# Kernel tuning notes

Measured on AMD Instinct MI355X. Metric: run time of the kernel, lower is better.

## Reference

```python
import jax, jax.numpy as jnp
import numpy as np

# dims
B, S, D, H, NB = 2, 2048, 1024, 16, 32
DH = D // H          # 64 per-head dim
MLP = 4096
CLUSTER_SCORE = 0.1
LN_EPS = 1e-6


def _layernorm(x, g, b):
    mu = jnp.mean(x, axis=-1, keepdims=True)
    var = jnp.mean(jnp.square(x - mu), axis=-1, keepdims=True)
    return (x - mu) * jax.lax.rsqrt(var + LN_EPS) * g + b


def setup_inputs() -> dict:
    key = jax.random.key(0)
    ks = jax.random.split(key, 10)
    std = 0.02  # xl_init-style normal init scale
    return {
        "inputs": jax.random.normal(ks[0], (B, S, D), jnp.float32),
        "ln1_g": jnp.ones((D,), jnp.float32),
        "ln1_b": jnp.zeros((D,), jnp.float32),
        "Wq": jax.random.normal(ks[1], (D, H, DH), jnp.float32) * std,
        "Wk": jax.random.normal(ks[2], (D, H, DH), jnp.float32) * std,
        "Wv": jax.random.normal(ks[3], (D, H, DH), jnp.float32) * std,
        "Whq": jax.random.normal(ks[4], (H, DH, NB), jnp.float32) * std,
        "Whk": jax.random.normal(ks[5], (H, DH, NB), jnp.float32) * std,
        "Wo": jax.random.normal(ks[6], (H, DH, D), jnp.float32) * std,
        "ln2_g": jnp.ones((D,), jnp.float32),
        "ln2_b": jnp.zeros((D,), jnp.float32),
        "W1": jax.random.normal(ks[7], (D, MLP), jnp.float32) * std,
        "b1": jnp.zeros((MLP,), jnp.float32),
        "W2": jax.random.normal(ks[8], (MLP, D), jnp.float32) * std,
        "b2": jnp.zeros((D,), jnp.float32),
    }


def _lha_attention(x, Wq, Wk, Wv, Whq, Whk, Wo):
    # q,k,v: [B,S,H,DH]
    q = jnp.einsum("bsd,dhf->bshf", x, Wq)
    k = jnp.einsum("bsd,dhf->bshf", x, Wk)
    v = jnp.einsum("bsd,dhf->bshf", x, Wv)
    # learned-hash bucket assignment probabilities (lha_score_func='linear')
    qb = jax.nn.softmax(jnp.einsum("bshf,hfn->bshn", q, Whq), axis=-1)  # [B,S,H,NB]
    kb = jax.nn.softmax(jnp.einsum("bshf,hfn->bshn", k, Whk), axis=-1)
    # content scores + cluster (same-bucket) affinity term
    logits = jnp.einsum("bqhf,bkhf->bhqk", q, k) / jnp.sqrt(jnp.float32(DH))
    aff = jnp.einsum("bqhn,bkhn->bhqk", qb, kb)  # [B,H,S,S]
    logits = logits + CLUSTER_SCORE * aff
    attn = jax.nn.softmax(logits, axis=-1)
    out = jnp.einsum("bhqk,bkhf->bqhf", attn, v)
    out = jnp.einsum("bqhf,hfd->bqd", out, Wo)
    # auxiliary bucket load-balancing loss
    mq = jnp.mean(qb, axis=(0, 1))  # [H,NB]
    mk = jnp.mean(kb, axis=(0, 1))
    extra_loss = 0.5 * NB * (jnp.mean(jnp.sum(mq * mq, -1)) + jnp.mean(jnp.sum(mk * mk, -1)))
    return out, extra_loss


def reference(inputs, ln1_g, ln1_b, Wq, Wk, Wv, Whq, Whk, Wo,
              ln2_g, ln2_b, W1, b1, W2, b2):
    x = _layernorm(inputs, ln1_g, ln1_b)                      # pre-LN
    attn_out, extra_loss = _lha_attention(x, Wq, Wk, Wv, Whq, Whk, Wo)
    x = attn_out + inputs                                      # residual
    y = _layernorm(x, ln2_g, ln2_b)                            # pre-LN for MLP
    y = jax.nn.relu(jnp.einsum("bsd,dm->bsm", y, W1) + b1)
    y = jnp.einsum("bsm,md->bsd", y, W2) + b2
    return (x + y, extra_loss)
```

## Files before the change

kernel.cpp:

```cpp
#include <hip/hip_runtime.h>

typedef unsigned short u16;
typedef unsigned int u32;
typedef float f32x4 __attribute__((ext_vector_type(4)));
typedef short bf16x8 __attribute__((ext_vector_type(8)));

#define D_B 2
#define D_S 2048
#define D_D 1024
#define D_H 16
#define D_NB 32
#define D_DH 64
#define D_MLP 4096

__device__ __forceinline__ float bflo(u32 p) { union { u32 i; float f; } c; c.i = p << 16; return c.f; }
__device__ __forceinline__ float bfhi(u32 p) { union { u32 i; float f; } c; c.i = p & 0xffff0000u; return c.f; }
__device__ __forceinline__ u16 f2bf(float f) {
  union { float f; u32 i; } c; c.f = f;
  u32 x = c.i;
  u32 r = (x + 0x7fffu + ((x >> 16) & 1u)) >> 16;
  return (u16)r;
}
__device__ __forceinline__ u32 pack2(float lo, float hi) {
  return (u32)f2bf(lo) | ((u32)f2bf(hi) << 16);
}
__device__ __forceinline__ void unpack8(uint4 u, float* f) {
  f[0]=bflo(u.x); f[1]=bfhi(u.x); f[2]=bflo(u.y); f[3]=bfhi(u.y);
  f[4]=bflo(u.z); f[5]=bfhi(u.z); f[6]=bflo(u.w); f[7]=bfhi(u.w);
}
__device__ __forceinline__ bf16x8 scale_frag(uint4 u, float s) {
  float f[8]; unpack8(u, f);
  uint4 r;
  r.x = pack2(f[0]*s, f[1]*s); r.y = pack2(f[2]*s, f[3]*s);
  r.z = pack2(f[4]*s, f[5]*s); r.w = pack2(f[6]*s, f[7]*s);
  union { uint4 u; bf16x8 v; } c; c.u = r; return c.v;
}
__device__ __forceinline__ bf16x8 as_frag(uint4 u) {
  union { uint4 u; bf16x8 v; } c; c.u = u; return c.v;
}
__device__ __forceinline__ void gl_lds16(const u16* g, u16* l) {
  __builtin_amdgcn_global_load_lds((const __attribute__((address_space(1))) void*)g,
                                   (__attribute__((address_space(3))) void*)l, 16, 0, 0);
}

__device__ __forceinline__ void tr64(const float* __restrict__ W, u16* __restrict__ WT,
                                     int K, int N, int k0, int n0, int t) {
  __shared__ float tile[64][65];
  int tx = t & 15, ty = t >> 4;
  #pragma unroll
  for (int i = 0; i < 4; i++) {
    float4 v = *reinterpret_cast<const float4*>(W + (size_t)(k0 + ty * 4 + i) * N + n0 + tx * 4);
    tile[ty * 4 + i][tx * 4 + 0] = v.x;
    tile[ty * 4 + i][tx * 4 + 1] = v.y;
    tile[ty * 4 + i][tx * 4 + 2] = v.z;
    tile[ty * 4 + i][tx * 4 + 3] = v.w;
  }
  __syncthreads();
  #pragma unroll
  for (int i = 0; i < 4; i++) {
    int n = ty * 4 + i;
    uint2 o;
    o.x = pack2(tile[tx*4+0][n], tile[tx*4+1][n]);
    o.y = pack2(tile[tx*4+2][n], tile[tx*4+3][n]);
    *reinterpret_cast<uint2*>(WT + (size_t)(n0 + n) * K + k0 + tx * 4) = o;
  }
}

__global__ __launch_bounds__(256) void prep1_kernel(const float* __restrict__ Wq,
                                                    const float* __restrict__ Wk,
                                                    const float* __restrict__ Wv,
                                                    const float* __restrict__ Wo,
                                                    u16* __restrict__ wqkvT,
                                                    u16* __restrict__ woT,
                                                    float* __restrict__ mqmk) {
  int bid = blockIdx.x, t = threadIdx.x;
  if (bid >= 1024) {
    reinterpret_cast<float4*>(mqmk)[t] = make_float4(0.f, 0.f, 0.f, 0.f);
    return;
  }
  const float* W; u16* WT;
  int sub = bid & 255;
  int k0 = (sub >> 4) * 64, n0 = (sub & 15) * 64;
  if (bid < 256)      { W = Wq; WT = wqkvT; }
  else if (bid < 512) { W = Wk; WT = wqkvT + 1024 * 1024; }
  else if (bid < 768) { W = Wv; WT = wqkvT + 2048 * 1024; }
  else                { W = Wo; WT = woT; }
  tr64(W, WT, 1024, 1024, k0, n0, t);
}

__global__ __launch_bounds__(256) void prep2_kernel(const float* __restrict__ W1,
                                                    const float* __restrict__ W2,
                                                    u16* __restrict__ w1T,
                                                    u16* __restrict__ w2T) {
  int bid = blockIdx.x, t = threadIdx.x;
  if (bid < 1024) {
    int n0 = (bid & 63) * 64, k0 = (bid >> 6) * 64;
    tr64(W1, w1T, 1024, 4096, k0, n0, t);
  } else {
    int i = bid - 1024;
    int n0 = (i & 15) * 64, k0 = (i >> 4) * 64;
    tr64(W2, w2T, 4096, 1024, k0, n0, t);
  }
}

__global__ __launch_bounds__(256) void ln_kernel(const float* __restrict__ x,
                                                 const float* __restrict__ g,
                                                 const float* __restrict__ bta,
                                                 u16* __restrict__ out) {
  int row = blockIdx.x, t = threadIdx.x;
  float4 v = reinterpret_cast<const float4*>(x + (size_t)row * D_D)[t];
  float s = v.x + v.y + v.z + v.w;
  float q = v.x*v.x + v.y*v.y + v.z*v.z + v.w*v.w;
  #pragma unroll
  for (int o = 32; o; o >>= 1) { s += __shfl_down(s, o); q += __shfl_down(q, o); }
  __shared__ float rs[4], rq[4];
  if ((t & 63) == 0) { rs[t >> 6] = s; rq[t >> 6] = q; }
  __syncthreads();
  s = rs[0] + rs[1] + rs[2] + rs[3];
  q = rq[0] + rq[1] + rq[2] + rq[3];
  float mu   = s * (1.0f / 1024.0f);
  float var  = fmaxf(q * (1.0f / 1024.0f) - mu * mu, 0.0f);
  float rstd = rsqrtf(var + 1e-6f);
  float4 gg = reinterpret_cast<const float4*>(g)[t];
  float4 bb = reinterpret_cast<const float4*>(bta)[t];
  float o0 = (v.x - mu) * rstd * gg.x + bb.x;
  float o1 = (v.y - mu) * rstd * gg.y + bb.y;
  float o2 = (v.z - mu) * rstd * gg.z + bb.z;
  float o3 = (v.w - mu) * rstd * gg.w + bb.w;
  uint2 w; w.x = pack2(o0, o1); w.y = pack2(o2, o3);
  reinterpret_cast<uint2*>(out + (size_t)row * D_D)[t] = w;
}

__global__ __launch_bounds__(256, 2) void gemm_bt(const u16* __restrict__ A,
                                                  const u16* __restrict__ Bt,
                                                  u16* __restrict__ Cq,
                                                  u16* __restrict__ Ck,
                                                  u16* __restrict__ Cv,
                                                  int M, int N, int K, int ldb) {
  __shared__ u16 As[128 * 32];
  __shared__ u16 Bs[128 * 32];
  const int t = threadIdx.x, w = t >> 6, lane = t & 63;
  const int quad = lane >> 4, l16 = lane & 15;
  const int m0 = blockIdx.y * 128, n0 = blockIdx.x * 128;
  const int wm = (w >> 1) * 64, wn = (w & 1) * 64;

  f32x4 acc[4][4];
  #pragma unroll
  for (int i = 0; i < 4; i++)
    #pragma unroll
    for (int n = 0; n < 4; n++) acc[i][n] = (f32x4){0.f, 0.f, 0.f, 0.f};

  const int srow = lane >> 2, scol = (lane & 3) * 8;
  const u16* ag0 = A  + (size_t)(m0 + w * 32 + srow) * K + scol;
  const u16* ag1 = ag0 + (size_t)16 * K;
  const u16* bg0 = Bt + (size_t)(n0 + w * 32 + srow) * ldb + scol;
  const u16* bg1 = bg0 + (size_t)16 * ldb;
  u16* al0 = As + w * 1024;
  u16* bl0 = Bs + w * 1024;

  for (int k0 = 0; k0 < K; k0 += 32) {
    gl_lds16(ag0 + k0, al0);
    gl_lds16(ag1 + k0, al0 + 512);
    gl_lds16(bg0 + k0, bl0);
    gl_lds16(bg1 + k0, bl0 + 512);
    __syncthreads();
    bf16x8 af[4], bf[4];
    #pragma unroll
    for (int i = 0; i < 4; i++)
      af[i] = *reinterpret_cast<const bf16x8*>(As + (wm + i * 16 + l16) * 32 + quad * 8);
    #pragma unroll
    for (int n = 0; n < 4; n++)
      bf[n] = *reinterpret_cast<const bf16x8*>(Bs + (wn + n * 16 + l16) * 32 + quad * 8);
    #pragma unroll
    for (int i = 0; i < 4; i++)
      #pragma unroll
      for (int n = 0; n < 4; n++)
        acc[i][n] = __builtin_amdgcn_mfma_f32_16x16x32_bf16(af[i], bf[n], acc[i][n], 0, 0, 0);
    __syncthreads();
  }

  #pragma unroll
  for (int i = 0; i < 4; i++) {
    #pragma unroll
    for (int r = 0; r < 4; r++) {
      const int m = m0 + wm + i * 16 + quad * 4 + r;
      #pragma unroll
      for (int nt = 0; nt < 4; nt++) {
        const int n = n0 + wn + nt * 16 + l16;
        float v = acc[i][nt][r];
        const int sel = n >> 10, nn = n & 1023;
        const int h = nn >> 6, f = nn & 63;
        const int b = m >> 11, s = m & 2047;
        const size_t bh = (size_t)(b * D_H + h);
        if (sel == 0)      Cq[(bh * D_S + s) * 96 + f] = f2bf(v);
        else if (sel == 1) Ck[(bh * D_S + s) * 96 + f] = f2bf(v);
        else               Cv[(bh * 64 + f) * D_S + s] = f2bf(v);
      }
    }
  }
}

__global__ __launch_bounds__(256, 2) void gemm_bt64(const u16* __restrict__ A,
                                                    const u16* __restrict__ Bt,
                                                    const float* __restrict__ bias,
                                                    const float* __restrict__ resid,
                                                    void* __restrict__ C,
                                                    int M, int N, int K, int ldb,
                                                    int do_relu, int out_f32) {
  __shared__ u16 As[64 * 32];
  __shared__ u16 Bs[128 * 32];
  const int t = threadIdx.x, w = t >> 6, lane = t & 63;
  const int quad = lane >> 4, l16 = lane & 15;
  const int m0 = blockIdx.y * 64, n0 = blockIdx.x * 128;
  const int wm = (w >> 1) * 32, wn = (w & 1) * 64;

  f32x4 acc[2][4];
  #pragma unroll
  for (int i = 0; i < 2; i++)
    #pragma unroll
    for (int n = 0; n < 4; n++) acc[i][n] = (f32x4){0.f, 0.f, 0.f, 0.f};

  const int srow = lane >> 2, scol = (lane & 3) * 8;
  const u16* ag0 = A  + (size_t)(m0 + w * 16 + srow) * K + scol;
  const u16* bg0 = Bt + (size_t)(n0 + w * 32 + srow) * ldb + scol;
  const u16* bg1 = bg0 + (size_t)16 * ldb;
  u16* al0 = As + w * 512;
  u16* bl0 = Bs + w * 1024;

  for (int k0 = 0; k0 < K; k0 += 32) {
    gl_lds16(ag0 + k0, al0);
    gl_lds16(bg0 + k0, bl0);
    gl_lds16(bg1 + k0, bl0 + 512);
    __syncthreads();
    bf16x8 af[2], bf[4];
    #pragma unroll
    for (int i = 0; i < 2; i++)
      af[i] = *reinterpret_cast<const bf16x8*>(As + (wm + i * 16 + l16) * 32 + quad * 8);
    #pragma unroll
    for (int n = 0; n < 4; n++)
      bf[n] = *reinterpret_cast<const bf16x8*>(Bs + (wn + n * 16 + l16) * 32 + quad * 8);
    #pragma unroll
    for (int i = 0; i < 2; i++)
      #pragma unroll
      for (int n = 0; n < 4; n++)
        acc[i][n] = __builtin_amdgcn_mfma_f32_16x16x32_bf16(af[i], bf[n], acc[i][n], 0, 0, 0);
    __syncthreads();
  }

  #pragma unroll
  for (int i = 0; i < 2; i++) {
    #pragma unroll
    for (int r = 0; r < 4; r++) {
      const int m = m0 + wm + i * 16 + quad * 4 + r;
      #pragma unroll
      for (int nt = 0; nt < 4; nt++) {
        const int n = n0 + wn + nt * 16 + l16;
        float v = acc[i][nt][r];
        if (bias)    v += bias[n];
        if (do_relu) v  = fmaxf(v, 0.0f);
        if (resid)   v += resid[(size_t)m * N + n];
        if (out_f32) reinterpret_cast<float*>(C)[(size_t)m * N + n] = v;
        else         reinterpret_cast<u16*>(C)[(size_t)m * N + n]   = f2bf(v);
      }
    }
  }
}

__global__ __launch_bounds__(256) void bucket2_kernel(u16* __restrict__ qp,
                                                      const float* __restrict__ Whq,
                                                      float* __restrict__ mq,
                                                      u16* __restrict__ kp,
                                                      const float* __restrict__ Whk,
                                                      float* __restrict__ mk) {
  const int bx = blockIdx.x;
  const int side = bx >> 8;
  u16* P        = side ? kp  : qp;
  const float* Wh = side ? Whk : Whq;
  float* acc    = side ? mk  : mq;
  const float sscale = side ? 1.0f : 0.1f;
  const int id = bx & 255;
  const int bh = id >> 3, chunk = id & 7;
  const int h = bh & 15;
  const int t = threadIdx.x, w = t >> 6, lane = t & 63;
  const int rsub = lane >> 5;
  const int b = lane & 31;

  __shared__ float WhL[32 * 65];
  __shared__ float qs[4][2][64];
  __shared__ float accL[32];

  #pragma unroll
  for (int i = 0; i < 8; i++) {
    int idx = t * 8 + i;
    WhL[(idx & 31) * 65 + (idx >> 5)] = Wh[h * 2048 + idx];
  }
  if (t < 32) accL[t] = 0.f;
  __syncthreads();

  float whr[64];
  #pragma unroll
  for (int i = 0; i < 16; i++) {
    float4 v = *reinterpret_cast<const float4*>(&WhL[b * 65 + i * 4]);
    whr[i*4+0] = v.x; whr[i*4+1] = v.y; whr[i*4+2] = v.z; whr[i*4+3] = v.w;
  }

  float racc = 0.f;
  const int row0 = bh * 2048 + chunk * 256;
  for (int it = 0; it < 32; it++) {
    const int rr = row0 + it * 8 + w * 2 + rsub;
    u16* qrow = P + (size_t)rr * 96;
    u32 u = *reinterpret_cast<const u32*>(qrow + b * 2);
    *reinterpret_cast<float2*>(&qs[w][rsub][b * 2]) = make_float2(bflo(u), bfhi(u));
    float s0 = 0.f, s1 = 0.f, s2 = 0.f, s3 = 0.f;
    #pragma unroll
    for (int i = 0; i < 16; i++) {
      float4 qv = *reinterpret_cast<const float4*>(&qs[w][rsub][i * 4]);
      s0 = fmaf(qv.x, whr[i*4+0], s0);
      s1 = fmaf(qv.y, whr[i*4+1], s1);
      s2 = fmaf(qv.z, whr[i*4+2], s2);
      s3 = fmaf(qv.w, whr[i*4+3], s3);
    }
    float l = (s0 + s1) + (s2 + s3);
    float m = l;
    m = fmaxf(m, __shfl_xor(m, 1));  m = fmaxf(m, __shfl_xor(m, 2));
    m = fmaxf(m, __shfl_xor(m, 4));  m = fmaxf(m, __shfl_xor(m, 8));
    m = fmaxf(m, __shfl_xor(m, 16));
    float e = __expf(fminf(l - m, 0.0f));
    float ss = e;
    ss += __shfl_xor(ss, 1);  ss += __shfl_xor(ss, 2);
    ss += __shfl_xor(ss, 4);  ss += __shfl_xor(ss, 8);
    ss += __shfl_xor(ss, 16);
    float p = e / fmaxf(ss, 1e-20f);
    qrow[64 + b] = f2bf(p * sscale);
    racc += p;
  }
  atomicAdd(&accL[b], racc);
  __syncthreads();
  if (t < 32) atomicAdd(&acc[h * D_NB + t], accL[t]);
}

__global__ __launch_bounds__(128, 2) void attn_kernel(const u16* __restrict__ qp,
                                                      const u16* __restrict__ kp,
                                                      const u16* __restrict__ vt,
                                                      u16* __restrict__ out) {
  const int bh = blockIdx.y;
  const int s0 = blockIdx.x * 64;
  const int h = bh & 15, b = bh >> 4;
  const int t = threadIdx.x, w = t >> 6, lane = t & 63;
  const int quad = lane >> 4, l16 = lane & 15;

  __shared__ u16 Ks[64 * 104];
  __shared__ u16 Vs[64 * 72];
  __shared__ u16 Ps[2][32 * 72];

  bf16x8 Qf[2][3];
  #pragma unroll
  for (int m = 0; m < 2; m++) {
    const u16* qr = qp + ((size_t)bh * D_S + s0 + w * 32 + m * 16 + l16) * 96;
    #pragma unroll
    for (int kg = 0; kg < 3; kg++) {
      uint4 u = *reinterpret_cast<const uint4*>(qr + kg * 32 + quad * 8);
      Qf[m][kg] = (kg < 2) ? scale_frag(u, 0.125f) : as_frag(u);
    }
  }

  f32x4 Oa[2][4];
  float lp[2][4];
  #pragma unroll
  for (int m = 0; m < 2; m++)
    #pragma unroll
    for (int f = 0; f < 4; f++) Oa[m][f] = (f32x4){0.f,0.f,0.f,0.f};
  #pragma unroll
  for (int m = 0; m < 2; m++)
    #pragma unroll
    for (int r = 0; r < 4; r++) lp[m][r] = 0.f;

  const int srow = t >> 1, shalf = t & 1;
  const u16* kgp = kp + ((size_t)bh * D_S + srow) * 96 + shalf * 48;
  const u16* vgp = vt + ((size_t)bh * 64 + srow) * D_S + shalf * 32;
  u16* kds = Ks + srow * 104 + shalf * 48;
  u16* vds = Vs + srow * 72 + shalf * 32;

  for (int kt = 0; kt < 32; kt++) {
    __syncthreads();
    {
      const u16* kg_ = kgp + (size_t)kt * 64 * 96;
      #pragma unroll
      for (int j = 0; j < 6; j++)
        *reinterpret_cast<uint4*>(kds + j * 8) = *reinterpret_cast<const uint4*>(kg_ + j * 8);
      const u16* vg_ = vgp + kt * 64;
      #pragma unroll
      for (int j = 0; j < 4; j++)
        *reinterpret_cast<uint4*>(vds + j * 8) = *reinterpret_cast<const uint4*>(vg_ + j * 8);
    }
    __syncthreads();

    f32x4 S[2][4];
    #pragma unroll
    for (int m = 0; m < 2; m++)
      #pragma unroll
      for (int n = 0; n < 4; n++) S[m][n] = (f32x4){0.f,0.f,0.f,0.f};
    #pragma unroll
    for (int n = 0; n < 4; n++) {
      bf16x8 Bk[3];
      #pragma unroll
      for (int kg = 0; kg < 3; kg++)
        Bk[kg] = *reinterpret_cast<const bf16x8*>(Ks + (n * 16 + l16) * 104 + kg * 32 + quad * 8);
      #pragma unroll
      for (int m = 0; m < 2; m++)
        #pragma unroll
        for (int kg = 0; kg < 3; kg++)
          S[m][n] = __builtin_amdgcn_mfma_f32_16x16x32_bf16(Qf[m][kg], Bk[kg], S[m][n], 0, 0, 0);
    }

    #pragma unroll
    for (int m = 0; m < 2; m++) {
      u16* pw = Ps[w] + (m * 16 + quad * 4) * 72 + l16;
      #pragma unroll
      for (int r = 0; r < 4; r++) {
        float es = 0.f;
        #pragma unroll
        for (int n = 0; n < 4; n++) {
          float e = __expf(fminf(S[m][n][r], 30.0f));
          es += e;
          pw[r * 72 + n * 16] = f2bf(e);
        }
        lp[m][r] += es;
      }
    }
    asm volatile("s_waitcnt lgkmcnt(0)" ::: "memory");

    #pragma unroll
    for (int m = 0; m < 2; m++) {
      bf16x8 Pa[2];
      #pragma unroll
      for (int kg = 0; kg < 2; kg++)
        Pa[kg] = *reinterpret_cast<const bf16x8*>(Ps[w] + (m * 16 + l16) * 72 + kg * 32 + quad * 8);
      #pragma unroll
      for (int f = 0; f < 4; f++)
        #pragma unroll
        for (int kg = 0; kg < 2; kg++) {
          bf16x8 Bv = *reinterpret_cast<const bf16x8*>(Vs + (f * 16 + l16) * 72 + kg * 32 + quad * 8);
          Oa[m][f] = __builtin_amdgcn_mfma_f32_16x16x32_bf16(Pa[kg], Bv, Oa[m][f], 0, 0, 0);
        }
    }
  }

  #pragma unroll
  for (int m = 0; m < 2; m++)
    #pragma unroll
    for (int r = 0; r < 4; r++) {
      float v = lp[m][r];
      v += __shfl_xor(v, 1); v += __shfl_xor(v, 2);
      v += __shfl_xor(v, 4); v += __shfl_xor(v, 8);
      float inv = 1.0f / fmaxf(v, 1e-20f);
      int qrow = s0 + w * 32 + m * 16 + quad * 4 + r;
      #pragma unroll
      for (int f = 0; f < 4; f++)
        out[((size_t)(b * D_S + qrow) * D_H + h) * 64 + f * 16 + l16] = f2bf(Oa[m][f][r] * inv);
    }
}

__global__ __launch_bounds__(256) void loss_kernel(const float* __restrict__ mq,
                                                   const float* __restrict__ mk,
                                                   float* __restrict__ out) {
  int t = threadIdx.x;
  float s = 0.0f;
  for (int i = t; i < 512; i += 256) {
    float a = mq[i] * (1.0f / 4096.0f);
    float c = mk[i] * (1.0f / 4096.0f);
    s += a * a + c * c;
  }
  #pragma unroll
  for (int o = 32; o; o >>= 1) s += __shfl_xor(s, o);
  __shared__ float r[4];
  if ((t & 63) == 0) r[t >> 6] = s;
  __syncthreads();
  if (t == 0) out[0] = r[0] + r[1] + r[2] + r[3];
}

extern "C" void kernel_launch(void* const* d_in, const int* in_sizes, int n_in,
                              void* d_out, int out_size, void* d_ws, size_t ws_size,
                              hipStream_t stream) {
  const float* inp  = (const float*)d_in[0];
  const float* ln1g = (const float*)d_in[1];
  const float* ln1b = (const float*)d_in[2];
  const float* Wq   = (const float*)d_in[3];
  const float* Wk   = (const float*)d_in[4];
  const float* Wv   = (const float*)d_in[5];
  const float* Whq  = (const float*)d_in[6];
  const float* Whk  = (const float*)d_in[7];
  const float* Wo   = (const float*)d_in[8];
  const float* ln2g = (const float*)d_in[9];
  const float* ln2b = (const float*)d_in[10];
  const float* W1   = (const float*)d_in[11];
  const float* b1   = (const float*)d_in[12];
  const float* W2   = (const float*)d_in[13];
  const float* b2   = (const float*)d_in[14];
  float* out = (float*)d_out;

  char* w = (char*)d_ws;
  u16* wqkvT = (u16*)(w + 0);
  u16* woT   = (u16*)(w + 6291456);
  u16* qp    = (u16*)(w + 8388608);
  u16* kp    = (u16*)(w + 20971520);
  u16* xhat  = (u16*)(w + 33554432);
  u16* attnb = xhat;
  float* mq  = (float*)(w + 41943040);
  float* mk  = mq + 512;
  u16* yhat  = (u16*)(w + 0);
  u16* w1T   = (u16*)(w + 8388608);
  u16* w2T   = (u16*)(w + 16777216);
  u16* h1    = (u16*)(w + 25165824);
  u16* vt    = (u16*)d_out;

  prep1_kernel<<<dim3(1025), dim3(256), 0, stream>>>(Wq, Wk, Wv, Wo, wqkvT, woT, mq);
  ln_kernel<<<dim3(4096), dim3(256), 0, stream>>>(inp, ln1g, ln1b, xhat);
  gemm_bt<<<dim3(24, 32), dim3(256), 0, stream>>>(xhat, wqkvT, qp, kp, vt, 4096, 3072, 1024, 1024);
  bucket2_kernel<<<dim3(512), dim3(256), 0, stream>>>(qp, Whq, mq, kp, Whk, mk);
  attn_kernel<<<dim3(32, 32), dim3(128), 0, stream>>>(qp, kp, vt, attnb);
  prep2_kernel<<<dim3(2048), dim3(256), 0, stream>>>(W1, W2, w1T, w2T);
  gemm_bt64<<<dim3(8, 64), dim3(256), 0, stream>>>(attnb, woT, nullptr, inp,
                                                   out, 4096, 1024, 1024, 1024, 0, 1);
  ln_kernel<<<dim3(4096), dim3(256), 0, stream>>>(out, ln2g, ln2b, yhat);
  gemm_bt64<<<dim3(16, 64), dim3(256), 0, stream>>>(yhat, w1T, b1, nullptr,
                                                    h1, 4096, 2048, 1024, 1024, 1, 0);
  gemm_bt64<<<dim3(8, 64), dim3(256), 0, stream>>>(h1, w2T, b2, out,
                                                   out, 4096, 1024, 2048, 4096, 0, 1);
  gemm_bt64<<<dim3(16, 64), dim3(256), 0, stream>>>(yhat, w1T + (size_t)2048 * 1024, b1 + 2048, nullptr,
                                                    h1, 4096, 2048, 1024, 1024, 1, 0);
  gemm_bt64<<<dim3(8, 64), dim3(256), 0, stream>>>(h1, w2T + 2048, nullptr, out,
                                                   out, 4096, 1024, 2048, 4096, 0, 1);
  loss_kernel<<<dim3(1), dim3(256), 0, stream>>>(mq, mk, out + 4194304);
}
```

Baseline: 487.1 us.

## Split attention KV range across two warp pairs and merge partial outputs

The attention block grows from 128 to 256 threads. Two extra waves process the second half of the key/value sequence in parallel with the first, using double K/V shared buffers, and their partial accumulators and row sums are merged through shared memory at the end. The P staging buffer gets a padded, swizzled layout to reduce LDS bank conflicts, and the bf16 conversion for P uses a cheaper round-half-up instead of round-to-nearest-even. The aim is more waves in flight per block to hide latency, at the cost of more shared memory per block, a final reduction step, and slightly different rounding of P.

Result: no change. 484.8 us (-0.5%).

```diff
diff --git a/kernel.cpp b/kernel.cpp
--- a/kernel.cpp
+++ b/kernel.cpp
@@ -20,6 +20,10 @@
   u32 x = c.i;
   u32 r = (x + 0x7fffu + ((x >> 16) & 1u)) >> 16;
   return (u16)r;
+}
+__device__ __forceinline__ u16 f2bf_fast(float f) {
+  union { float f; u32 i; } c; c.f = f;
+  return (u16)((c.i + 0x8000u) >> 16);
 }
 __device__ __forceinline__ u32 pack2(float lo, float hi) {
   return (u32)f2bf(lo) | ((u32)f2bf(hi) << 16);
@@ -339,7 +343,7 @@
   if (t < 32) atomicAdd(&acc[h * D_NB + t], accL[t]);
 }
 
-__global__ __launch_bounds__(128, 2) void attn_kernel(const u16* __restrict__ qp,
+__global__ __launch_bounds__(256, 2) void attn_kernel(const u16* __restrict__ qp,
                                                       const u16* __restrict__ kp,
                                                       const u16* __restrict__ vt,
                                                       u16* __restrict__ out) {
@@ -348,15 +352,17 @@
   const int h = bh & 15, b = bh >> 4;
   const int t = threadIdx.x, w = t >> 6, lane = t & 63;
   const int quad = lane >> 4, l16 = lane & 15;
-
-  __shared__ u16 Ks[64 * 104];
-  __shared__ u16 Vs[64 * 72];
-  __shared__ u16 Ps[2][32 * 72];
+  const int qh = w & 1, kvh = w >> 1;
+
+  __shared__ u16 Ks[2][64 * 104];
+  __shared__ u16 Vs[2][64 * 72];
+  __shared__ u16 Ps[4][32 * 88];
+  __shared__ float Lb[64];
 
   bf16x8 Qf[2][3];
   #pragma unroll
   for (int m = 0; m < 2; m++) {
-    const u16* qr = qp + ((size_t)bh * D_S + s0 + w * 32 + m * 16 + l16) * 96;
+    const u16* qr = qp + ((size_t)bh * D_S + s0 + qh * 32 + m * 16 + l16) * 96;
     #pragma unroll
     for (int kg = 0; kg < 3; kg++) {
       uint4 u = *reinterpret_cast<const uint4*>(qr + kg * 32 + quad * 8);
@@ -375,23 +381,31 @@
     #pragma unroll
     for (int r = 0; r < 4; r++) lp[m][r] = 0.f;
 
-  const int srow = t >> 1, shalf = t & 1;
-  const u16* kgp = kp + ((size_t)bh * D_S + srow) * 96 + shalf * 48;
-  const u16* vgp = vt + ((size_t)bh * 64 + srow) * D_S + shalf * 32;
-  u16* kds = Ks + srow * 104 + shalf * 48;
-  u16* vds = Vs + srow * 72 + shalf * 32;
-
-  for (int kt = 0; kt < 32; kt++) {
+  const int srow = t >> 2, seg = t & 3;
+  const u16* kgp = kp + ((size_t)bh * D_S + srow) * 96 + seg * 24;
+  const u16* vgp = vt + ((size_t)bh * 64 + srow) * D_S + seg * 16;
+  u16* kd0 = &Ks[0][srow * 104 + seg * 24];
+  u16* kd1 = &Ks[1][srow * 104 + seg * 24];
+  u16* vd0 = &Vs[0][srow * 72 + seg * 16];
+  u16* vd1 = &Vs[1][srow * 72 + seg * 16];
+
+  for (int kt = 0; kt < 16; kt++) {
     __syncthreads();
     {
-      const u16* kg_ = kgp + (size_t)kt * 64 * 96;
-      #pragma unroll
-      for (int j = 0; j < 6; j++)
-        *reinterpret_cast<uint4*>(kds + j * 8) = *reinterpret_cast<const uint4*>(kg_ + j * 8);
-      const u16* vg_ = vgp + kt * 64;
-      #pragma unroll
-      for (int j = 0; j < 4; j++)
-        *reinterpret_cast<uint4*>(vds + j * 8) = *reinterpret_cast<const uint4*>(vg_ + j * 8);
+      const u16* ka = kgp + (size_t)(kt * 64) * 96;
+      const u16* kb = kgp + (size_t)(1024 + kt * 64) * 96;
+      #pragma unroll
+      for (int j = 0; j < 3; j++) {
+        *reinterpret_cast<uint4*>(kd0 + j * 8) = *reinterpret_cast<const uint4*>(ka + j * 8);
+        *reinterpret_cast<uint4*>(kd1 + j * 8) = *reinterpret_cast<const uint4*>(kb + j * 8);
+      }
+      const u16* va = vgp + kt * 64;
+      const u16* vb = vgp + 1024 + kt * 64;
+      #pragma unroll
+      for (int j = 0; j < 2; j++) {
+        *reinterpret_cast<uint4*>(vd0 + j * 8) = *reinterpret_cast<const uint4*>(va + j * 8);
+        *reinterpret_cast<uint4*>(vd1 + j * 8) = *reinterpret_cast<const uint4*>(vb + j * 8);
+      }
     }
     __syncthreads();
 
@@ -405,7 +419,7 @@
       bf16x8 Bk[3];
       #pragma unroll
       for (int kg = 0; kg < 3; kg++)
-        Bk[kg] = *reinterpret_cast<const bf16x8*>(Ks + (n * 16 + l16) * 104 + kg * 32 + quad * 8);
+        Bk[kg] = *reinterpret_cast<const bf16x8*>(&Ks[kvh][(n * 16 + l16) * 104 + kg * 32 + quad * 8]);
       #pragma unroll
       for (int m = 0; m < 2; m++)
         #pragma unroll
@@ -415,15 +429,16 @@
 
     #pragma unroll
     for (int m = 0; m < 2; m++) {
-      u16* pw = Ps[w] + (m * 16 + quad * 4) * 72 + l16;
       #pragma unroll
       for (int r = 0; r < 4; r++) {
+        const int row = m * 16 + quad * 4 + r;
+        u16* pw = &Ps[w][row * 88 + ((row >> 3) & 1) * 16 + l16];
         float es = 0.f;
         #pragma unroll
         for (int n = 0; n < 4; n++) {
           float e = __expf(fminf(S[m][n][r], 30.0f));
           es += e;
-          pw[r * 72 + n * 16] = f2bf(e);
+          pw[n * 16] = f2bf_fast(e);
         }
         lp[m][r] += es;
       }
@@ -432,20 +447,22 @@
 
     #pragma unroll
     for (int m = 0; m < 2; m++) {
+      const int row = m * 16 + l16;
       bf16x8 Pa[2];
       #pragma unroll
       for (int kg = 0; kg < 2; kg++)
-        Pa[kg] = *reinterpret_cast<const bf16x8*>(Ps[w] + (m * 16 + l16) * 72 + kg * 32 + quad * 8);
+        Pa[kg] = *reinterpret_cast<const bf16x8*>(&Ps[w][row * 88 + ((row >> 3) & 1) * 16 + kg * 32 + quad * 8]);
       #pragma unroll
       for (int f = 0; f < 4; f++)
         #pragma unroll
         for (int kg = 0; kg < 2; kg++) {
-          bf16x8 Bv = *reinterpret_cast<const bf16x8*>(Vs + (f * 16 + l16) * 72 + kg * 32 + quad * 8);
+          bf16x8 Bv = *reinterpret_cast<const bf16x8*>(&Vs[kvh][(f * 16 + l16) * 72 + kg * 32 + quad * 8]);
           Oa[m][f] = __builtin_amdgcn_mfma_f32_16x16x32_bf16(Pa[kg], Bv, Oa[m][f], 0, 0, 0);
         }
     }
   }
 
+  float lpr[2][4];
   #pragma unroll
   for (int m = 0; m < 2; m++)
     #pragma unroll
@@ -453,12 +470,39 @@
       float v = lp[m][r];
       v += __shfl_xor(v, 1); v += __shfl_xor(v, 2);
       v += __shfl_xor(v, 4); v += __shfl_xor(v, 8);
-      float inv = 1.0f / fmaxf(v, 1e-20f);
-      int qrow = s0 + w * 32 + m * 16 + quad * 4 + r;
-      #pragma unroll
-      for (int f = 0; f < 4; f++)
-        out[((size_t)(b * D_S + qrow) * D_H + h) * 64 + f * 16 + l16] = f2bf(Oa[m][f][r] * inv);
-    }
+      lpr[m][r] = v;
+    }
+
+  __syncthreads();
+  float* Ob = reinterpret_cast<float*>(&Ks[0][0]);
+  if (kvh == 1) {
+    #pragma unroll
+    for (int m = 0; m < 2; m++)
+      #pragma unroll
+      for (int r = 0; r < 4; r++) {
+        const int row = qh * 32 + m * 16 + quad * 4 + r;
+        if (l16 == 0) Lb[row] = lpr[m][r];
+        #pragma unroll
+        for (int f = 0; f < 4; f++)
+          Ob[row * 68 + f * 16 + l16] = Oa[m][f][r];
+      }
+  }
+  __syncthreads();
+  if (kvh == 0) {
+    #pragma unroll
+    for (int m = 0; m < 2; m++)
+      #pragma unroll
+      for (int r = 0; r < 4; r++) {
+        const int row = qh * 32 + m * 16 + quad * 4 + r;
+        float ltot = lpr[m][r] + Lb[row];
+        float inv = 1.0f / fmaxf(ltot, 1e-20f);
+        #pragma unroll
+        for (int f = 0; f < 4; f++) {
+          float val = (Oa[m][f][r] + Ob[row * 68 + f * 16 + l16]) * inv;
+          out[((size_t)(b * D_S + s0 + row) * D_H + h) * 64 + f * 16 + l16] = f2bf(val);
+        }
+      }
+  }
 }
 
 __global__ __launch_bounds__(256) void loss_kernel(const float* __restrict__ mq,
@@ -518,7 +562,7 @@
   ln_kernel<<<dim3(4096), dim3(256), 0, stream>>>(inp, ln1g, ln1b, xhat);
   gemm_bt<<<dim3(24, 32), dim3(256), 0, stream>>>(xhat, wqkvT, qp, kp, vt, 4096, 3072, 1024, 1024);
   bucket2_kernel<<<dim3(512), dim3(256), 0, stream>>>(qp, Whq, mq, kp, Whk, mk);
-  attn_kernel<<<dim3(32, 32), dim3(128), 0, stream>>>(qp, kp, vt, attnb);
+  attn_kernel<<<dim3(32, 32), dim3(256), 0, stream>>>(qp, kp, vt, attnb);
   prep2_kernel<<<dim3(2048), dim3(256), 0, stream>>>(W1, W2, w1T, w2T);
   gemm_bt64<<<dim3(8, 64), dim3(256), 0, stream>>>(attnb, woT, nullptr, inp,
                                                    out, 4096, 1024, 1024, 1024, 0, 1);
```
